# Kernel optimization log

Hardware: AMD Instinct MI355X
Metric: run time of the kernel (lower is better)

The kernel has to match this reference:

```python
import jax, jax.numpy as jnp
import numpy as np

L, D, DH, NH, P = 12, 768, 64, 12, 16
B, H_IMG, W_IMG = 16, 384, 384
MAX_GRID = 64


def setup_inputs() -> dict:
    key = jax.random.key(0)
    ks = jax.random.split(key, 10)
    r = lambda k, shp: (0.02 * jax.random.normal(k, shp, dtype=jnp.float32))
    return {
        "x": jax.random.normal(ks[0], (B, 3, H_IMG, W_IMG), dtype=jnp.float32),
        "conv_w": r(ks[1], (D, 3, P, P)),
        "conv_b": jnp.zeros((D,), jnp.float32),
        "ln_w": jnp.ones((D,), jnp.float32),
        "ln_b": jnp.zeros((D,), jnp.float32),
        "pos_y_emb": r(ks[2], (MAX_GRID, D)),
        "pos_x_emb": r(ks[3], (MAX_GRID, D)),
        "mha_ln_w": jnp.ones((L, D), jnp.float32),
        "mha_ln_b": jnp.zeros((L, D), jnp.float32),
        "qw": r(ks[4], (L, D, D)),
        "kw": r(ks[5], (L, D, D)),
        "vw": r(ks[6], (L, D, D)),
        "ffn_ln_w": jnp.ones((L, D), jnp.float32),
        "ffn_ln_b": jnp.zeros((L, D), jnp.float32),
        "w1": r(ks[7], (L, D, 4 * D)),
        "b1": jnp.zeros((L, 4 * D), jnp.float32),
        "w2": r(ks[8], (L, 4 * D, D)),
        "b2": jnp.zeros((L, D), jnp.float32),
        "x_shift": 0,
        "y_shift": 0,
    }


def _ln(x, w, b):
    m = jnp.mean(x, axis=-1, keepdims=True)
    v = jnp.var(x, axis=-1, keepdims=True)
    return (x - m) * jax.lax.rsqrt(v + 1e-5) * w + b


def reference(x, conv_w, conv_b, ln_w, ln_b, pos_y_emb, pos_x_emb,
              mha_ln_w, mha_ln_b, qw, kw, vw,
              ffn_ln_w, ffn_ln_b, w1, b1, w2, b2, x_shift, y_shift):
    # patch embed: conv + relu, to NHWC, layernorm
    h = jax.lax.conv_general_dilated(x, conv_w, (P, P), 'VALID',
                                     dimension_numbers=('NCHW', 'OIHW', 'NCHW'))
    h = jax.nn.relu(h + conv_b[None, :, None, None])
    h = jnp.transpose(h, (0, 2, 3, 1))  # [B, GH, GW, D]
    h = _ln(h, ln_w, ln_b)
    b, gh, gw, d = h.shape
    n = gh * gw
    # 2D factorized positional embedding, shared layernorm
    pos = (pos_y_emb[jnp.arange(gh) + y_shift][:, None, :]
           + pos_x_emb[jnp.arange(gw) + x_shift][None, :, :])  # [GH, GW, D]
    pos = _ln(pos, ln_w, ln_b).reshape(1, n, d)
    pos_emb = jnp.broadcast_to(pos, (b, n, d))
    t = h.reshape(b, n, d) + pos_emb
    scale = 1.0 / jnp.sqrt(jnp.float32(DH))
    for i in range(L):
        # pre-LN MHA (no output projection, mask=None / pretrain=False)
        tl = _ln(t, mha_ln_w[i], mha_ln_b[i])
        q = (tl @ qw[i]).reshape(b, n, NH, DH).transpose(0, 2, 1, 3)
        k = (tl @ kw[i]).reshape(b, n, NH, DH).transpose(0, 2, 1, 3)
        v = (tl @ vw[i]).reshape(b, n, NH, DH).transpose(0, 2, 1, 3)
        attn = jax.nn.softmax(jnp.einsum('bhqd,bhkd->bhqk', q, k) * scale, axis=-1)
        o = jnp.einsum('bhqk,bhkd->bhqd', attn, v).transpose(0, 2, 1, 3).reshape(b, n, d)
        t = t + o
        fl = _ln(t, ffn_ln_w[i], ffn_ln_b[i])
        t = t + (jax.nn.relu(fl @ w1[i] + b1[i]) @ w2[i] + b2[i])
    return t, pos_emb
```

## Files before the change

kernel.cpp:

```cpp
#include <hip/hip_runtime.h>

typedef unsigned short u16;
typedef __attribute__((ext_vector_type(4))) float f32x4;
typedef __attribute__((ext_vector_type(8))) short s16x8;

__device__ __forceinline__ u16 f2bf(float f) {
    union { float f; unsigned u; } v; v.f = f;
    unsigned r = v.u + 0x7FFFu + ((v.u >> 16) & 1u);
    return (u16)(r >> 16);
}

__device__ __forceinline__ void gload_lds16(const u16* g, u16* l) {
    __builtin_amdgcn_global_load_lds(
        (const __attribute__((address_space(1))) unsigned int*)(g),
        (__attribute__((address_space(3))) unsigned int*)(l),
        16, 0, 0);
}

#define NTOK 9216
#define SEQ  576
#define DMODEL 768
#define DFF  3072
#define NHEAD 12
#define HDIM 64

__global__ __launch_bounds__(256) void convert_bf16_kernel(const float* __restrict__ in,
                                                           u16* __restrict__ out, int n) {
    for (int i = blockIdx.x * 256 + threadIdx.x; i < n; i += gridDim.x * 256)
        out[i] = f2bf(in[i]);
}

__global__ __launch_bounds__(256) void copy_f32_kernel(const float* __restrict__ in,
                                                       float* __restrict__ out, int n4) {
    const float4* a = (const float4*)in;
    float4* o = (float4*)out;
    for (int i = blockIdx.x * 256 + threadIdx.x; i < n4; i += gridDim.x * 256)
        o[i] = a[i];
}

__global__ __launch_bounds__(256) void im2col_kernel(const float* __restrict__ x,
                                                     u16* __restrict__ out) {
    int tok = blockIdx.x;
    int b = tok / SEQ, n = tok % SEQ;
    int gy = n / 24, gx = n % 24;
    int tid = threadIdx.x;
#pragma unroll
    for (int j = 0; j < 3; ++j) {
        int col = tid + j * 256;
        int c = col >> 8, py = (col >> 4) & 15, px = col & 15;
        float v = x[(size_t)((b * 3 + c) * 384 + gy * 16 + py) * 384 + gx * 16 + px];
        out[(size_t)tok * DMODEL + col] = f2bf(v);
    }
}

__global__ __launch_bounds__(256) void transpose64_kernel(
        const float* __restrict__ qw0, const float* __restrict__ kw0, const float* __restrict__ vw0,
        const float* __restrict__ w10, const float* __restrict__ w20,
        u16* __restrict__ wTqkv0, u16* __restrict__ w1T0, u16* __restrict__ w2T0,
        size_t wqkv_stride, size_t w1_stride) {
    int layer = blockIdx.x / 1584;
    int bid = blockIdx.x % 1584;
    const float* qw = qw0 + (size_t)layer * 768 * 768;
    const float* kw = kw0 + (size_t)layer * 768 * 768;
    const float* vw = vw0 + (size_t)layer * 768 * 768;
    const float* w1 = w10 + (size_t)layer * 768 * DFF;
    const float* w2 = w20 + (size_t)layer * DFF * 768;
    u16* wTq = wTqkv0 + (size_t)layer * wqkv_stride;
    u16* wTk = wTq + (size_t)768 * 768;
    u16* wTv = wTq + (size_t)2 * 768 * 768;
    u16* w1T = w1T0 + (size_t)layer * w1_stride;
    u16* w2T = w2T0 + (size_t)layer * w1_stride;

    const float* src; u16* dst; int Kd, Nd, tile;
    if (bid < 432)       { int m = bid / 144; src = m == 0 ? qw : (m == 1 ? kw : vw);
                           dst = m == 0 ? wTq : (m == 1 ? wTk : wTv); Kd = 768; Nd = 768; tile = bid % 144; }
    else if (bid < 1008) { src = w1; dst = w1T; Kd = 768; Nd = 3072; tile = bid - 432; }
    else                 { src = w2; dst = w2T; Kd = 3072; Nd = 768; tile = bid - 1008; }
    int ntx = Nd >> 6;
    int tk = (tile / ntx) << 6, tn = (tile % ntx) << 6;
    __shared__ float ts[64][65];
    int tx4 = threadIdx.x & 15, ty = threadIdx.x >> 4;
#pragma unroll
    for (int j = 0; j < 64; j += 16) {
        float4 v = *(const float4*)&src[(size_t)(tk + ty + j) * Nd + tn + tx4 * 4];
        ts[ty + j][tx4 * 4 + 0] = v.x;
        ts[ty + j][tx4 * 4 + 1] = v.y;
        ts[ty + j][tx4 * 4 + 2] = v.z;
        ts[ty + j][tx4 * 4 + 3] = v.w;
    }
    __syncthreads();
    int kx = threadIdx.x & 31, ry = threadIdx.x >> 5;
#pragma unroll
    for (int j = 0; j < 64; j += 8) {
        int r = ry + j;
        unsigned lo = f2bf(ts[2 * kx][r]);
        unsigned hi = f2bf(ts[2 * kx + 1][r]);
        *(unsigned*)&dst[(size_t)(tn + r) * Kd + tk + 2 * kx] = lo | (hi << 16);
    }
}

__global__ __launch_bounds__(256) void ln_bf16_kernel(const float* __restrict__ X,
                                                      const float* __restrict__ w,
                                                      const float* __restrict__ b,
                                                      u16* __restrict__ Y) {
    int row = blockIdx.x, tid = threadIdx.x;
    const float* x = X + (size_t)row * DMODEL;
    float v0 = x[tid], v1 = x[tid + 256], v2 = x[tid + 512];
    float s = v0 + v1 + v2, sq = v0 * v0 + v1 * v1 + v2 * v2;
#pragma unroll
    for (int off = 32; off >= 1; off >>= 1) { s += __shfl_down(s, off); sq += __shfl_down(sq, off); }
    __shared__ float red[8];
    if ((tid & 63) == 0) { red[tid >> 6] = s; red[4 + (tid >> 6)] = sq; }
    __syncthreads();
    float S = red[0] + red[1] + red[2] + red[3];
    float Q = red[4] + red[5] + red[6] + red[7];
    float mean = S * (1.f / DMODEL);
    float var = Q * (1.f / DMODEL) - mean * mean;
    float inv = rsqrtf(var + 1e-5f);
    u16* y = Y + (size_t)row * DMODEL;
    y[tid]       = f2bf((v0 - mean) * inv * w[tid]       + b[tid]);
    y[tid + 256] = f2bf((v1 - mean) * inv * w[tid + 256] + b[tid + 256]);
    y[tid + 512] = f2bf((v2 - mean) * inv * w[tid + 512] + b[tid + 512]);
}

__global__ __launch_bounds__(256) void ln_add_pos_kernel(float* __restrict__ T,
                                                         const float* __restrict__ w,
                                                         const float* __restrict__ b,
                                                         const float* __restrict__ posln) {
    int row = blockIdx.x, tid = threadIdx.x;
    float* x = T + (size_t)row * DMODEL;
    const float* p = posln + (size_t)(row % SEQ) * DMODEL;
    float v0 = x[tid], v1 = x[tid + 256], v2 = x[tid + 512];
    float s = v0 + v1 + v2, sq = v0 * v0 + v1 * v1 + v2 * v2;
#pragma unroll
    for (int off = 32; off >= 1; off >>= 1) { s += __shfl_down(s, off); sq += __shfl_down(sq, off); }
    __shared__ float red[8];
    if ((tid & 63) == 0) { red[tid >> 6] = s; red[4 + (tid >> 6)] = sq; }
    __syncthreads();
    float S = red[0] + red[1] + red[2] + red[3];
    float Q = red[4] + red[5] + red[6] + red[7];
    float mean = S * (1.f / DMODEL);
    float var = Q * (1.f / DMODEL) - mean * mean;
    float inv = rsqrtf(var + 1e-5f);
    x[tid]       = (v0 - mean) * inv * w[tid]       + b[tid]       + p[tid];
    x[tid + 256] = (v1 - mean) * inv * w[tid + 256] + b[tid + 256] + p[tid + 256];
    x[tid + 512] = (v2 - mean) * inv * w[tid + 512] + b[tid + 512] + p[tid + 512];
}

__global__ __launch_bounds__(256) void pos_ln_kernel(const float* __restrict__ py,
                                                     const float* __restrict__ px,
                                                     const float* __restrict__ w,
                                                     const float* __restrict__ b,
                                                     const int* __restrict__ xs_p,
                                                     const int* __restrict__ ys_p,
                                                     float* __restrict__ posln,
                                                     float* __restrict__ out2) {
    int row = blockIdx.x;
    int gy = row / 24, gx = row % 24;
    int ys = ys_p[0], xs = xs_p[0];
    int tid = threadIdx.x;
    float v[3]; float s = 0.f, sq = 0.f;
#pragma unroll
    for (int j = 0; j < 3; ++j) {
        int c = tid + j * 256;
        v[j] = py[(size_t)(gy + ys) * DMODEL + c] + px[(size_t)(gx + xs) * DMODEL + c];
        s += v[j]; sq += v[j] * v[j];
    }
#pragma unroll
    for (int off = 32; off >= 1; off >>= 1) { s += __shfl_down(s, off); sq += __shfl_down(sq, off); }
    __shared__ float red[8];
    if ((tid & 63) == 0) { red[tid >> 6] = s; red[4 + (tid >> 6)] = sq; }
    __syncthreads();
    float S = red[0] + red[1] + red[2] + red[3];
    float Q = red[4] + red[5] + red[6] + red[7];
    float mean = S * (1.f / DMODEL);
    float var = Q * (1.f / DMODEL) - mean * mean;
    float inv = rsqrtf(var + 1e-5f);
#pragma unroll
    for (int j = 0; j < 3; ++j) {
        int c = tid + j * 256;
        float y = (v[j] - mean) * inv * w[c] + b[c];
        posln[(size_t)row * DMODEL + c] = y;
        for (int bb = 0; bb < 16; ++bb)
            out2[((size_t)bb * SEQ + row) * DMODEL + c] = y;
    }
}

#define EPI_CONV 0
#define EPI_QKV  1
#define EPI_FFN1 3
#define EPI_FFN2 4

template <int EPI>
__global__ __launch_bounds__(512, 4) void gemm3b(const u16* __restrict__ A,
                                                 const u16* __restrict__ Bt,
                                                 float* __restrict__ outF,
                                                 u16* __restrict__ outB,
                                                 u16* __restrict__ outB2,
                                                 u16* __restrict__ outB3,
                                                 const float* __restrict__ bias,
                                                 int lda, int N, int K) {
    __shared__ __align__(16) u16 lds[3 * 12288];
    const int tid = threadIdx.x;
    const int wave = tid >> 6, lane = tid & 63;
    const int c_lo = lane & 15, c_hi = lane >> 4;
    const int wm = wave >> 2, wn = wave & 3;
    const int m0 = blockIdx.x * 128, n0 = blockIdx.y * 256;
    const int NT = K >> 5;

    const int srow = tid >> 2;
    const int koff = ((tid & 3) * 8) ^ (((srow >> 1) & 3) << 3);
    const u16* pA = A  + (size_t)(m0 + srow) * lda + koff;
    const u16* pB = Bt + (size_t)(n0 + srow) * lda + koff;
    const size_t rstepB = (size_t)128 * lda;
    f32x4 acc[4][4] = {};

    auto stage = [&](int t) {
        u16* buf = lds + (t % 3) * 12288;
        int k0 = t << 5;
        gload_lds16(pA + k0, buf + tid * 8);
        gload_lds16(pB + k0, buf + 4096 + tid * 8);
        gload_lds16(pB + rstepB + k0, buf + 8192 + tid * 8);
    };

    stage(0); stage(1);
    asm volatile("s_waitcnt vmcnt(3)" ::: "memory");
    __builtin_amdgcn_s_barrier();
    __builtin_amdgcn_sched_barrier(0);

    const int sw = ((c_lo >> 1) & 3) << 3;
    const int colA = (c_hi * 8) ^ sw;

    for (int t = 0; t < NT; ++t) {
        if (t + 2 < NT) stage(t + 2);
        const u16* buf = lds + (t % 3) * 12288;
        s16x8 af[4], bf[4];
#pragma unroll
        for (int m = 0; m < 4; ++m)
            af[m] = *(const s16x8*)(buf + (wm * 64 + m * 16 + c_lo) * 32 + colA);
#pragma unroll
        for (int n = 0; n < 4; ++n)
            bf[n] = *(const s16x8*)(buf + 4096 + (wn * 64 + n * 16 + c_lo) * 32 + colA);
        asm volatile("s_waitcnt lgkmcnt(0)" ::: "memory");
        __builtin_amdgcn_sched_barrier(0);
        __builtin_amdgcn_s_setprio(1);
#pragma unroll
        for (int m = 0; m < 4; ++m)
#pragma unroll
            for (int n = 0; n < 4; ++n)
                acc[m][n] = __builtin_amdgcn_mfma_f32_16x16x32_bf16(af[m], bf[n], acc[m][n], 0, 0, 0);
        __builtin_amdgcn_s_setprio(0);
        if (t + 2 < NT)      { asm volatile("s_waitcnt vmcnt(3)" ::: "memory"); }
        else if (t + 1 < NT) { asm volatile("s_waitcnt vmcnt(0)" ::: "memory"); }
        __builtin_amdgcn_s_barrier();
        __builtin_amdgcn_sched_barrier(0);
    }

#pragma unroll
    for (int mf = 0; mf < 4; ++mf)
#pragma unroll
        for (int nf = 0; nf < 4; ++nf) {
            int gcol = n0 + wn * 64 + nf * 16 + c_lo;
            int tb = m0 + wm * 64 + mf * 16 + c_hi * 4;
            if (EPI == EPI_QKV && (n0 / 768) == 2) {
                int lcol = gcol - 2 * 768;
                int b = tb / SEQ, nt = tb % SEQ;
                int h = lcol >> 6, dh = lcol & 63;
                unsigned long long pk =
                    (unsigned long long)f2bf(acc[mf][nf][0])
                    | ((unsigned long long)f2bf(acc[mf][nf][1]) << 16)
                    | ((unsigned long long)f2bf(acc[mf][nf][2]) << 32)
                    | ((unsigned long long)f2bf(acc[mf][nf][3]) << 48);
                *(unsigned long long*)&outB3[(size_t)(((b * NHEAD + h) << 6) + dh) * SEQ + nt] = pk;
                continue;
            }
#pragma unroll
            for (int rr = 0; rr < 4; ++rr) {
                int grow = tb + rr;
                float v = acc[mf][nf][rr];
                if (EPI == EPI_CONV) {
                    v += bias[gcol]; v = fmaxf(v, 0.f);
                    outF[(size_t)grow * 768 + gcol] = v;
                } else if (EPI == EPI_QKV) {
                    int sel = n0 / 768;
                    int lcol = gcol - sel * 768;
                    if (sel == 0)      outB [(size_t)grow * 768 + lcol] = f2bf(v);
                    else               outB2[(size_t)grow * 768 + lcol] = f2bf(v);
                } else if (EPI == EPI_FFN1) {
                    v += bias[gcol]; v = fmaxf(v, 0.f);
                    outB[(size_t)grow * N + gcol] = f2bf(v);
                } else if (EPI == EPI_FFN2) {
                    outF[(size_t)grow * 768 + gcol] += v + bias[gcol];
                }
            }
        }
}

__global__ __launch_bounds__(256) void attn_kernel(const u16* __restrict__ Qb,
                                                   const u16* __restrict__ Kb,
                                                   const u16* __restrict__ Vt,
                                                   float* __restrict__ T) {
    int bid = blockIdx.x;
    int qt = bid / 192, bh = bid % 192;
    int b = bh / NHEAD, h = bh % NHEAD;
    int q0 = qt * 64;
    const int tid = threadIdx.x, wave = tid >> 6, lane = tid & 63;
    const int c_lo = lane & 15, c_hi = lane >> 4;
    __shared__ __align__(16) u16 Qs[64][72];
    __shared__ __align__(16) u16 Ks[64][72];
    __shared__ __align__(16) u16 Vs[64][72];
    __shared__ __align__(16) u16 Ps[4][16][72];
#pragma unroll
    for (int i = 0; i < 2; ++i) {
        int c = i * 256 + tid, row = c >> 3, slot = (c & 7) * 8;
        *(s16x8*)&Qs[row][slot] =
            *(const s16x8*)(Qb + ((size_t)(b * SEQ + q0 + row) * DMODEL + h * HDIM + slot));
    }
    s16x8 kreg[2], vreg[2];
    {
#pragma unroll
        for (int i = 0; i < 2; ++i) {
            int c = i * 256 + tid, row = c >> 3, slot = (c & 7) * 8;
            kreg[i] = *(const s16x8*)(Kb + ((size_t)(b * SEQ + row) * DMODEL + h * HDIM + slot));
            vreg[i] = *(const s16x8*)(Vt + ((size_t)((b * NHEAD + h) * HDIM + row) * SEQ + slot));
        }
    }
    f32x4 o[4] = {};
    float mrun[4], lrun[4];
#pragma unroll
    for (int r = 0; r < 4; ++r) { mrun[r] = -1e30f; lrun[r] = 0.f; }
    for (int t2 = 0; t2 < 9; ++t2) {
        __builtin_amdgcn_s_barrier();
#pragma unroll
        for (int i = 0; i < 2; ++i) {
            int c = i * 256 + tid, row = c >> 3, slot = (c & 7) * 8;
            *(s16x8*)&Ks[row][slot] = kreg[i];
            *(s16x8*)&Vs[row][slot] = vreg[i];
        }
        asm volatile("s_waitcnt lgkmcnt(0)" ::: "memory");
        __builtin_amdgcn_s_barrier();
        __builtin_amdgcn_sched_barrier(0);
        if (t2 < 8) {
            int kv0 = (t2 + 1) * 64;
#pragma unroll
            for (int i = 0; i < 2; ++i) {
                int c = i * 256 + tid, row = c >> 3, slot = (c & 7) * 8;
                kreg[i] = *(const s16x8*)(Kb + ((size_t)(b * SEQ + kv0 + row) * DMODEL + h * HDIM + slot));
                vreg[i] = *(const s16x8*)(Vt + ((size_t)((b * NHEAD + h) * HDIM + row) * SEQ + kv0 + slot));
            }
        }
        f32x4 s[4] = {};
        s16x8 aq[2];
#pragma unroll
        for (int ks = 0; ks < 2; ++ks)
            aq[ks] = *(const s16x8*)&Qs[wave * 16 + c_lo][ks * 32 + c_hi * 8];
#pragma unroll
        for (int nf = 0; nf < 4; ++nf)
#pragma unroll
            for (int ks = 0; ks < 2; ++ks) {
                s16x8 bk = *(const s16x8*)&Ks[nf * 16 + c_lo][ks * 32 + c_hi * 8];
                s[nf] = __builtin_amdgcn_mfma_f32_16x16x32_bf16(aq[ks], bk, s[nf], 0, 0, 0);
            }
#pragma unroll
        for (int nf = 0; nf < 4; ++nf)
#pragma unroll
            for (int r = 0; r < 4; ++r) s[nf][r] *= 0.125f;
        float mx[4];
#pragma unroll
        for (int r = 0; r < 4; ++r)
            mx[r] = fmaxf(fmaxf(s[0][r], s[1][r]), fmaxf(s[2][r], s[3][r]));
#pragma unroll
        for (int off = 1; off < 16; off <<= 1)
#pragma unroll
            for (int r = 0; r < 4; ++r) mx[r] = fmaxf(mx[r], __shfl_xor(mx[r], off));
        float alpha[4];
#pragma unroll
        for (int r = 0; r < 4; ++r) {
            float mn = fmaxf(mrun[r], mx[r]);
            alpha[r] = __expf(mrun[r] - mn);
            mrun[r] = mn;
            lrun[r] *= alpha[r];
        }
        float ls[4] = {0.f, 0.f, 0.f, 0.f};
        u16 pb[4][4];
#pragma unroll
        for (int nf = 0; nf < 4; ++nf)
#pragma unroll
            for (int r = 0; r < 4; ++r) {
                float p = __expf(s[nf][r] - mrun[r]);
                ls[r] += p;
                pb[nf][r] = f2bf(p);
            }
#pragma unroll
        for (int off = 1; off < 16; off <<= 1)
#pragma unroll
            for (int r = 0; r < 4; ++r) ls[r] += __shfl_xor(ls[r], off);
#pragma unroll
        for (int r = 0; r < 4; ++r) lrun[r] += ls[r];
#pragma unroll
        for (int df = 0; df < 4; ++df)
#pragma unroll
            for (int r = 0; r < 4; ++r) o[df][r] *= alpha[r];
#pragma unroll
        for (int nf = 0; nf < 4; ++nf)
#pragma unroll
            for (int r = 0; r < 4; ++r)
                Ps[wave][c_hi * 4 + r][c_lo + nf * 16] = pb[nf][r];
        asm volatile("s_waitcnt lgkmcnt(0)" ::: "memory");
        s16x8 pa[2];
#pragma unroll
        for (int ks = 0; ks < 2; ++ks)
            pa[ks] = *(const s16x8*)&Ps[wave][c_lo][ks * 32 + c_hi * 8];
#pragma unroll
        for (int df = 0; df < 4; ++df)
#pragma unroll
            for (int ks = 0; ks < 2; ++ks) {
                s16x8 bv = *(const s16x8*)&Vs[df * 16 + c_lo][ks * 32 + c_hi * 8];
                o[df] = __builtin_amdgcn_mfma_f32_16x16x32_bf16(pa[ks], bv, o[df], 0, 0, 0);
            }
    }
#pragma unroll
    for (int df = 0; df < 4; ++df)
#pragma unroll
        for (int r = 0; r < 4; ++r) {
            int grow = b * SEQ + q0 + wave * 16 + c_hi * 4 + r;
            int gcol = h * HDIM + df * 16 + c_lo;
            T[(size_t)grow * DMODEL + gcol] += o[df][r] / lrun[r];
        }
}

extern "C" void kernel_launch(void* const* d_in, const int* in_sizes, int n_in,
                              void* d_out, int out_size, void* d_ws, size_t ws_size,
                              hipStream_t stream) {
    (void)in_sizes; (void)n_in; (void)out_size;
    const float* x        = (const float*)d_in[0];
    const float* conv_w   = (const float*)d_in[1];
    const float* conv_b   = (const float*)d_in[2];
    const float* ln_w     = (const float*)d_in[3];
    const float* ln_b     = (const float*)d_in[4];
    const float* pos_y    = (const float*)d_in[5];
    const float* pos_x    = (const float*)d_in[6];
    const float* mha_ln_w = (const float*)d_in[7];
    const float* mha_ln_b = (const float*)d_in[8];
    const float* qw       = (const float*)d_in[9];
    const float* kw       = (const float*)d_in[10];
    const float* vw       = (const float*)d_in[11];
    const float* ffn_ln_w = (const float*)d_in[12];
    const float* ffn_ln_b = (const float*)d_in[13];
    const float* w1       = (const float*)d_in[14];
    const float* b1       = (const float*)d_in[15];
    const float* w2       = (const float*)d_in[16];
    const float* b2       = (const float*)d_in[17];
    const int*   xs       = (const int*)d_in[18];
    const int*   ys       = (const int*)d_in[19];
    float* out1 = (float*)d_out;
    float* out2 = out1 + (size_t)NTOK * DMODEL;

    size_t off = 0;
    char* ws = (char*)d_ws;
    auto carve = [&](size_t bytes) { char* p = ws + off; off += (bytes + 255) & ~(size_t)255; return p; };
    float* t  = (float*)carve((size_t)NTOK * DMODEL * 4);
    u16* tl   = (u16*)carve((size_t)NTOK * DMODEL * 2);
    u16* qb   = (u16*)carve((size_t)NTOK * DMODEL * 2);
    u16* kb   = (u16*)carve((size_t)NTOK * DMODEL * 2);
    u16* vT   = (u16*)carve((size_t)NTOK * DMODEL * 2);
    u16* hb   = (u16*)carve((size_t)NTOK * DFF * 2);
    float* posln = (float*)carve((size_t)SEQ * DMODEL * 4);
    const size_t QKV_STRIDE = (size_t)3 * 768 * 768;
    const size_t W1_STRIDE  = (size_t)768 * DFF;
    size_t need_all = off + (QKV_STRIDE + 2 * W1_STRIDE) * 12 * 2 + 4096;
    bool hoist = (ws_size >= need_all);
    int nl = hoist ? 12 : 1;
    u16* wTqkv = (u16*)carve(QKV_STRIDE * nl * 2);
    u16* w1T   = (u16*)carve(W1_STRIDE * nl * 2);
    u16* w2T   = (u16*)carve(W1_STRIDE * nl * 2);
    u16* cw    = wTqkv;
    u16* im2c  = hb;

    convert_bf16_kernel<<<1152, 256, 0, stream>>>(conv_w, cw, 768 * 768);
    im2col_kernel<<<NTOK, 256, 0, stream>>>(x, im2c);
    gemm3b<EPI_CONV><<<dim3(72, 3), 512, 0, stream>>>(im2c, cw, t, nullptr, nullptr, nullptr,
                                                      conv_b, 768, 768, 768);
    pos_ln_kernel<<<SEQ, 256, 0, stream>>>(pos_y, pos_x, ln_w, ln_b, xs, ys, posln, out2);
    ln_add_pos_kernel<<<NTOK, 256, 0, stream>>>(t, ln_w, ln_b, posln);
    if (hoist)
        transpose64_kernel<<<1584 * 12, 256, 0, stream>>>(qw, kw, vw, w1, w2,
                                                          wTqkv, w1T, w2T, QKV_STRIDE, W1_STRIDE);

    for (int i = 0; i < 12; ++i) {
        if (!hoist)
            transpose64_kernel<<<1584, 256, 0, stream>>>(
                qw + (size_t)i * 768 * 768, kw + (size_t)i * 768 * 768, vw + (size_t)i * 768 * 768,
                w1 + (size_t)i * 768 * DFF, w2 + (size_t)i * DFF * 768,
                wTqkv, w1T, w2T, 0, 0);
        u16* wq = wTqkv + (hoist ? (size_t)i * QKV_STRIDE : 0) * 1;
        u16* wf1 = w1T + (hoist ? (size_t)i * W1_STRIDE : 0);
        u16* wf2 = w2T + (hoist ? (size_t)i * W1_STRIDE : 0);
        ln_bf16_kernel<<<NTOK, 256, 0, stream>>>(t, mha_ln_w + i * DMODEL, mha_ln_b + i * DMODEL, tl);
        gemm3b<EPI_QKV><<<dim3(72, 9), 512, 0, stream>>>(tl, wq, nullptr, qb, kb, vT,
                                                         nullptr, 768, 2304, 768);
        attn_kernel<<<16 * NHEAD * 9, 256, 0, stream>>>(qb, kb, vT, t);
        ln_bf16_kernel<<<NTOK, 256, 0, stream>>>(t, ffn_ln_w + i * DMODEL, ffn_ln_b + i * DMODEL, tl);
        gemm3b<EPI_FFN1><<<dim3(72, 12), 512, 0, stream>>>(tl, wf1, nullptr, hb, nullptr, nullptr,
                                                           b1 + (size_t)i * DFF, 768, 3072, 768);
        gemm3b<EPI_FFN2><<<dim3(72, 3), 512, 0, stream>>>(hb, wf2, t, nullptr, nullptr, nullptr,
                                                          b2 + (size_t)i * DMODEL, 3072, 768, 3072);
    }
    copy_f32_kernel<<<2048, 256, 0, stream>>>(t, out1, (NTOK * DMODEL) / 4);
}
```

Baseline: 3.110 ms.

## Add 64-row-tile GEMM for conv and FFN2, fuse final output copy

Introduces a new gemm64 kernel with 64x256 tiles, a triple-buffered LDS pipeline fed by direct global-to-LDS loads, and higher occupancy (launch bounds 512,4). The N=768 GEMMs (patch conv and FFN2) use it with a 144x3 grid instead of 72x3, so the grid fills more compute units. The final layer's FFN2 epilogue also writes the result straight to the output buffer, removing the separate full-tensor copy kernel. The cost is less operand reuse per tile and more kernel code to maintain.

```diff
diff --git a/kernel.cpp b/kernel.cpp
--- a/kernel.cpp
+++ b/kernel.cpp
@@ -28,14 +28,6 @@
                                                            u16* __restrict__ out, int n) {
     for (int i = blockIdx.x * 256 + threadIdx.x; i < n; i += gridDim.x * 256)
         out[i] = f2bf(in[i]);
-}
-
-__global__ __launch_bounds__(256) void copy_f32_kernel(const float* __restrict__ in,
-                                                       float* __restrict__ out, int n4) {
-    const float4* a = (const float4*)in;
-    float4* o = (float4*)out;
-    for (int i = blockIdx.x * 256 + threadIdx.x; i < n4; i += gridDim.x * 256)
-        o[i] = a[i];
 }
 
 __global__ __launch_bounds__(256) void im2col_kernel(const float* __restrict__ x,
@@ -278,10 +270,7 @@
             for (int rr = 0; rr < 4; ++rr) {
                 int grow = tb + rr;
                 float v = acc[mf][nf][rr];
-                if (EPI == EPI_CONV) {
-                    v += bias[gcol]; v = fmaxf(v, 0.f);
-                    outF[(size_t)grow * 768 + gcol] = v;
-                } else if (EPI == EPI_QKV) {
+                if (EPI == EPI_QKV) {
                     int sel = n0 / 768;
                     int lcol = gcol - sel * 768;
                     if (sel == 0)      outB [(size_t)grow * 768 + lcol] = f2bf(v);
@@ -289,11 +278,96 @@
                 } else if (EPI == EPI_FFN1) {
                     v += bias[gcol]; v = fmaxf(v, 0.f);
                     outB[(size_t)grow * N + gcol] = f2bf(v);
+                }
+            }
+        }
+}
+
+template <int EPI>
+__global__ __launch_bounds__(512, 4) void gemm64(const u16* __restrict__ A,
+                                                 const u16* __restrict__ Bt,
+                                                 float* __restrict__ outF,
+                                                 float* __restrict__ outDup,
+                                                 const float* __restrict__ bias,
+                                                 int lda, int K) {
+    __shared__ __align__(16) u16 lds[3 * 10240];
+    const int tid = threadIdx.x;
+    const int wave = tid >> 6, lane = tid & 63;
+    const int c_lo = lane & 15, c_hi = lane >> 4;
+    const int m0 = blockIdx.x * 64, n0 = blockIdx.y * 256;
+    const int NT = K >> 5;
+
+    const int srow = tid >> 2;
+    const int koff = ((tid & 3) * 8) ^ (((srow >> 1) & 3) << 3);
+    const u16* pA = A  + (size_t)(m0 + (srow & 63)) * lda + koff;
+    const u16* pB = Bt + (size_t)(n0 + srow) * lda + koff;
+    const size_t rstepB = (size_t)128 * lda;
+    f32x4 acc[4][2] = {};
+
+    auto stage = [&](int t) {
+        u16* buf = lds + (t % 3) * 10240;
+        int k0 = t << 5;
+        if (tid < 256) gload_lds16(pA + k0, buf + tid * 8);
+        gload_lds16(pB + k0, buf + 2048 + tid * 8);
+        gload_lds16(pB + rstepB + k0, buf + 6144 + tid * 8);
+    };
+
+    stage(0); stage(1);
+    if (wave < 4) { asm volatile("s_waitcnt vmcnt(3)" ::: "memory"); }
+    else          { asm volatile("s_waitcnt vmcnt(2)" ::: "memory"); }
+    __builtin_amdgcn_s_barrier();
+    __builtin_amdgcn_sched_barrier(0);
+
+    const int colA = (c_hi * 8) ^ (((c_lo >> 1) & 3) << 3);
+
+    for (int t = 0; t < NT; ++t) {
+        if (t + 2 < NT) stage(t + 2);
+        const u16* buf = lds + (t % 3) * 10240;
+        s16x8 af[4], bf[2];
+#pragma unroll
+        for (int m = 0; m < 4; ++m)
+            af[m] = *(const s16x8*)(buf + (m * 16 + c_lo) * 32 + colA);
+#pragma unroll
+        for (int n = 0; n < 2; ++n)
+            bf[n] = *(const s16x8*)(buf + 2048 + (wave * 32 + n * 16 + c_lo) * 32 + colA);
+        asm volatile("s_waitcnt lgkmcnt(0)" ::: "memory");
+        __builtin_amdgcn_sched_barrier(0);
+        __builtin_amdgcn_s_setprio(1);
+#pragma unroll
+        for (int m = 0; m < 4; ++m)
+#pragma unroll
+            for (int n = 0; n < 2; ++n)
+                acc[m][n] = __builtin_amdgcn_mfma_f32_16x16x32_bf16(af[m], bf[n], acc[m][n], 0, 0, 0);
+        __builtin_amdgcn_s_setprio(0);
+        if (t + 2 < NT) {
+            if (wave < 4) { asm volatile("s_waitcnt vmcnt(3)" ::: "memory"); }
+            else          { asm volatile("s_waitcnt vmcnt(2)" ::: "memory"); }
+        } else if (t + 1 < NT) {
+            asm volatile("s_waitcnt vmcnt(0)" ::: "memory");
+        }
+        __builtin_amdgcn_s_barrier();
+        __builtin_amdgcn_sched_barrier(0);
+    }
+
+#pragma unroll
+    for (int mf = 0; mf < 4; ++mf)
+#pragma unroll
+        for (int nf = 0; nf < 2; ++nf)
+#pragma unroll
+            for (int rr = 0; rr < 4; ++rr) {
+                int grow = m0 + mf * 16 + c_hi * 4 + rr;
+                int gcol = n0 + wave * 32 + nf * 16 + c_lo;
+                float v = acc[mf][nf][rr];
+                if (EPI == EPI_CONV) {
+                    v += bias[gcol]; v = fmaxf(v, 0.f);
+                    outF[(size_t)grow * 768 + gcol] = v;
                 } else if (EPI == EPI_FFN2) {
-                    outF[(size_t)grow * 768 + gcol] += v + bias[gcol];
+                    size_t idx = (size_t)grow * 768 + gcol;
+                    float nv = outF[idx] + v + bias[gcol];
+                    outF[idx] = nv;
+                    if (outDup) outDup[idx] = nv;
                 }
             }
-        }
 }
 
 __global__ __launch_bounds__(256) void attn_kernel(const u16* __restrict__ Qb,
@@ -479,8 +553,7 @@
 
     convert_bf16_kernel<<<1152, 256, 0, stream>>>(conv_w, cw, 768 * 768);
     im2col_kernel<<<NTOK, 256, 0, stream>>>(x, im2c);
-    gemm3b<EPI_CONV><<<dim3(72, 3), 512, 0, stream>>>(im2c, cw, t, nullptr, nullptr, nullptr,
-                                                      conv_b, 768, 768, 768);
+    gemm64<EPI_CONV><<<dim3(144, 3), 512, 0, stream>>>(im2c, cw, t, nullptr, conv_b, 768, 768);
     pos_ln_kernel<<<SEQ, 256, 0, stream>>>(pos_y, pos_x, ln_w, ln_b, xs, ys, posln, out2);
     ln_add_pos_kernel<<<NTOK, 256, 0, stream>>>(t, ln_w, ln_b, posln);
     if (hoist)
@@ -493,7 +566,7 @@
                 qw + (size_t)i * 768 * 768, kw + (size_t)i * 768 * 768, vw + (size_t)i * 768 * 768,
                 w1 + (size_t)i * 768 * DFF, w2 + (size_t)i * DFF * 768,
                 wTqkv, w1T, w2T, 0, 0);
-        u16* wq = wTqkv + (hoist ? (size_t)i * QKV_STRIDE : 0) * 1;
+        u16* wq  = wTqkv + (hoist ? (size_t)i * QKV_STRIDE : 0);
         u16* wf1 = w1T + (hoist ? (size_t)i * W1_STRIDE : 0);
         u16* wf2 = w2T + (hoist ? (size_t)i * W1_STRIDE : 0);
         ln_bf16_kernel<<<NTOK, 256, 0, stream>>>(t, mha_ln_w + i * DMODEL, mha_ln_b + i * DMODEL, tl);
@@ -503,8 +576,8 @@
         ln_bf16_kernel<<<NTOK, 256, 0, stream>>>(t, ffn_ln_w + i * DMODEL, ffn_ln_b + i * DMODEL, tl);
         gemm3b<EPI_FFN1><<<dim3(72, 12), 512, 0, stream>>>(tl, wf1, nullptr, hb, nullptr, nullptr,
                                                            b1 + (size_t)i * DFF, 768, 3072, 768);
-        gemm3b<EPI_FFN2><<<dim3(72, 3), 512, 0, stream>>>(hb, wf2, t, nullptr, nullptr, nullptr,
-                                                          b2 + (size_t)i * DMODEL, 3072, 768, 3072);
-    }
-    copy_f32_kernel<<<2048, 256, 0, stream>>>(t, out1, (NTOK * DMODEL) / 4);
-}
+        gemm64<EPI_FFN2><<<dim3(144, 3), 512, 0, stream>>>(hb, wf2, t,
+                                                           (i == 11) ? out1 : nullptr,
+                                                           b2 + (size_t)i * DMODEL, 3072, 3072);
+    }
+}
```

After: 3.375 ms. +8.5%, slower.
